# Optimization experiments

Hardware: AMD Instinct MI355X
Metric: run time of the kernel (lower is better)

Reference implementation:

```python
import jax, jax.numpy as jnp
import numpy as np

EMBED_DIM = 768
NUM_HEADS = 12
HEAD_DIM = EMBED_DIM // NUM_HEADS
B, S = 2, 2048


def setup_inputs() -> dict:
    key = jax.random.key(0)
    ks = jax.random.split(key, 6)
    glorot = jnp.sqrt(6.0 / (EMBED_DIM + EMBED_DIM)).astype(jnp.float32)
    x = jax.random.normal(ks[0], (B, S, EMBED_DIM), dtype=jnp.float32)
    mask = jnp.zeros((1, 1, S, S), dtype=jnp.float32)  # additive mask, 0 = no masking
    Wq = jax.random.uniform(ks[1], (EMBED_DIM, EMBED_DIM), jnp.float32, -glorot, glorot)
    Wk = jax.random.uniform(ks[2], (EMBED_DIM, EMBED_DIM), jnp.float32, -glorot, glorot)
    Wv = jax.random.uniform(ks[3], (EMBED_DIM, EMBED_DIM), jnp.float32, -glorot, glorot)
    Wo = jax.random.uniform(ks[4], (EMBED_DIM, EMBED_DIM), jnp.float32, -glorot, glorot)
    bo = jnp.zeros((EMBED_DIM,), dtype=jnp.float32)
    return {"x": x, "mask": mask, "Wq": Wq, "Wk": Wk, "Wv": Wv, "Wo": Wo, "bo": bo}


def reference(x, mask, Wq, Wk, Wv, Wo, bo):
    b, s, _ = x.shape
    # Q/K/V projections (no bias), split into heads: [b, h, s, d]
    def split_heads(t):
        return t.reshape(b, s, NUM_HEADS, HEAD_DIM).transpose(0, 2, 1, 3)
    q = split_heads(x @ Wq)
    k = split_heads(x @ Wk)
    v = split_heads(x @ Wv)
    scale = 1.0 / jnp.sqrt(jnp.float32(HEAD_DIM))
    logits = jnp.einsum('bhqd,bhkd->bhqk', q, k) * scale  # [b, h, s, s]
    logits = logits + mask * (-1e9)
    weights = jax.nn.softmax(logits, axis=-1)
    attn = jnp.einsum('bhqk,bhkd->bhqd', weights, v)
    concat = attn.transpose(0, 2, 1, 3).reshape(b, s, EMBED_DIM)
    return concat @ Wo + bo
```

## Files before the change

kernel.cpp:

```cpp
#include <hip/hip_runtime.h>


typedef __bf16 bf16_t;
typedef bf16_t bf16x8 __attribute__((ext_vector_type(8)));
typedef bf16_t bf16x4 __attribute__((ext_vector_type(4)));
typedef float f32x4 __attribute__((ext_vector_type(4)));
typedef _Float16 f16x4 __attribute__((ext_vector_type(4)));
typedef __fp16 hf2 __attribute__((ext_vector_type(2)));

#define SC2 0.1803368801111137f

__device__ __forceinline__ float bf2f(unsigned short u) {
  union { unsigned int i; float f; } x;
  x.i = ((unsigned int)u) << 16;
  return x.f;
}

__device__ __forceinline__ float fexp2(float x) {
  return __builtin_amdgcn_exp2f(x);
}

__device__ __forceinline__ void glds16(const bf16_t* g, bf16_t* l) {
  __builtin_amdgcn_global_load_lds(
      (const __attribute__((address_space(1))) void*)g,
      (__attribute__((address_space(3))) void*)l, 16, 0, 0);
}

__device__ __forceinline__ int detect_bf16_flag(const unsigned short* x) {
  const int lane = threadIdx.x & 63;
  const uint4* p = (const uint4*)x;
  uint4 a = p[lane * 2];
  uint4 b = p[lane * 2 + 1];
  unsigned int w[8] = {a.x, a.y, a.z, a.w, b.x, b.y, b.z, b.w};
  unsigned int big = 0;
#pragma unroll
  for (int i = 0; i < 8; i++) {
    unsigned int e0 = (w[i] >> 7) & 0xFF, e1 = (w[i] >> 23) & 0xFF;
    big |= (e0 > 0x88u) | (e1 > 0x88u);
  }
  unsigned long long bal = __ballot(big != 0u);
  return bal == 0ULL ? 1 : 0;
}

__global__ void k_prep(const void* __restrict__ x, const void* __restrict__ mask,
                       const void* __restrict__ Wq, const void* __restrict__ Wk,
                       const void* __restrict__ Wv, const void* __restrict__ Wo,
                       bf16_t* __restrict__ xb, bf16_t* __restrict__ wqkvT,
                       bf16_t* __restrict__ woT, int* __restrict__ mflags) {
  __shared__ float ts[32][33];
  __shared__ int snz;
  const int blk = blockIdx.x;
  const int f = detect_bf16_flag((const unsigned short*)x);

  if (blk < 1536) {
    if (f) return;
    int i = blk * 256 + threadIdx.x;
    const float* xf = (const float*)x + (size_t)i * 8;
    bf16x8 v;
#pragma unroll
    for (int j = 0; j < 8; j++) v[j] = (bf16_t)xf[j];
    *(bf16x8*)(xb + (size_t)i * 8) = v;
  } else if (blk < 3840) {
    const int t = blk - 1536;
    const int z = t / 576, r = t % 576, kt = r / 24, nt = r % 24;
    const void* wsrc = (z == 0) ? Wq : (z == 1) ? Wk : (z == 2) ? Wv : Wo;
    bf16_t* dst = (z < 3) ? (wqkvT + (size_t)z * 768 * 768) : woT;
    const int c = threadIdx.x & 31, r0 = threadIdx.x >> 5;
#pragma unroll
    for (int i = 0; i < 4; i++) {
      int kr = kt * 32 + r0 + i * 8;
      float v;
      if (f) v = bf2f(((const unsigned short*)wsrc)[(size_t)kr * 768 + nt * 32 + c]);
      else   v = ((const float*)wsrc)[(size_t)kr * 768 + nt * 32 + c];
      ts[r0 + i * 8][c] = v;
    }
    __syncthreads();
#pragma unroll
    for (int i = 0; i < 4; i++) {
      int nr = nt * 32 + r0 + i * 8;
      dst[(size_t)nr * 768 + kt * 32 + c] = (bf16_t)ts[c][r0 + i * 8];
    }
  } else {
    const int t = blk - 3840;
    const int qt = t >> 4, ktm = t & 15;
    if (threadIdx.x == 0) snz = 0;
    __syncthreads();
    unsigned int nz = 0;
    if (f) {
#pragma unroll
      for (int i = 0; i < 8; i++) {
        int uidx = i * 256 + threadIdx.x;
        int row = uidx >> 4, col = uidx & 15;
        const uint4* p = (const uint4*)((const char*)mask +
            ((size_t)(qt * 128 + row) * 2048 + ktm * 128) * 2 + col * 16);
        uint4 v = *p;
        nz |= ((v.x | v.y | v.z | v.w) & 0x7fff7fffu);
      }
    } else {
#pragma unroll
      for (int i = 0; i < 16; i++) {
        int uidx = i * 256 + threadIdx.x;
        int row = uidx >> 5, col = uidx & 31;
        const uint4* p = (const uint4*)((const char*)mask +
            ((size_t)(qt * 128 + row) * 2048 + ktm * 128) * 4 + col * 16);
        uint4 v = *p;
        nz |= ((v.x | v.y | v.z | v.w) & 0x7fffffffu);
      }
    }
    if (nz) snz = 1;
    __syncthreads();
    if (threadIdx.x == 0) mflags[qt * 16 + ktm] = snz;
  }
}

__global__ __launch_bounds__(256, 3) void k_gemmQKV(
    const bf16_t* __restrict__ xb, const bf16_t* __restrict__ Bm,
    bf16_t* __restrict__ Qd, bf16_t* __restrict__ Kd, _Float16* __restrict__ Vt,
    const unsigned short* __restrict__ xdet) {
  __shared__ __align__(16) char smem[32768];
  _Float16* Tb = (_Float16*)smem;

  const int f = detect_bf16_flag(xdet);
  const bf16_t* A = f ? (const bf16_t*)xdet : xb;

  const int tid = threadIdx.x;
  const int n0 = blockIdx.x * 128, m0 = blockIdx.y * 128;
  const int r = tid >> 2, c8 = (tid & 3) << 3;
  const bf16_t* Ag = A + (size_t)(m0 + r) * 768 + c8;
  const bf16_t* Bg = Bm + (size_t)(n0 + r) * 768 + c8;
  const int wid = tid >> 6, lane = tid & 63;
  const int wm = (wid >> 1) << 6, wn = (wid & 1) << 6;
  const int lr = lane & 15, lk = (lane >> 4) << 3, g4 = (lane >> 4) << 2;

  f32x4 acc[4][4];
  const f32x4 z = {0.f, 0.f, 0.f, 0.f};
#pragma unroll
  for (int i = 0; i < 4; i++)
#pragma unroll
    for (int j = 0; j < 4; j++) acc[i][j] = z;

  {
    bf16_t* A0 = (bf16_t*)smem;
    bf16_t* B0 = (bf16_t*)(smem + 16384);
    glds16(Ag, A0 + wid * 512);
    glds16(Ag + (size_t)64 * 768, A0 + 2048 + wid * 512);
    glds16(Bg, B0 + wid * 512);
    glds16(Bg + (size_t)64 * 768, B0 + 2048 + wid * 512);
  }
  __syncthreads();

  for (int s = 0; s < 24; s++) {
    if (s < 23) {
      const int k0 = (s + 1) * 32;
      bf16_t* An = (bf16_t*)(smem + ((s + 1) & 1) * 8192);
      bf16_t* Bn = (bf16_t*)(smem + 16384 + ((s + 1) & 1) * 8192);
      glds16(Ag + k0, An + wid * 512);
      glds16(Ag + (size_t)64 * 768 + k0, An + 2048 + wid * 512);
      glds16(Bg + k0, Bn + wid * 512);
      glds16(Bg + (size_t)64 * 768 + k0, Bn + 2048 + wid * 512);
    }
    const bf16_t* As = (const bf16_t*)(smem + (s & 1) * 8192);
    const bf16_t* Bs = (const bf16_t*)(smem + 16384 + (s & 1) * 8192);
    bf16x8 af[4], bf_[4];
#pragma unroll
    for (int t = 0; t < 4; t++) af[t]  = *(const bf16x8*)&As[(wm + t * 16 + lr) * 32 + lk];
#pragma unroll
    for (int t = 0; t < 4; t++) bf_[t] = *(const bf16x8*)&Bs[(wn + t * 16 + lr) * 32 + lk];
#pragma unroll
    for (int i = 0; i < 4; i++)
#pragma unroll
      for (int j = 0; j < 4; j++)
        acc[i][j] = __builtin_amdgcn_mfma_f32_16x16x32_bf16(af[i], bf_[j], acc[i][j], 0, 0, 0);
    __syncthreads();
  }

  if (n0 < 1536) {
    bf16_t* dst = (n0 < 768) ? Qd : Kd;
    const int nb = (n0 < 768) ? n0 : n0 - 768;
    const int bb = m0 >> 11;
#pragma unroll
    for (int i = 0; i < 4; i++)
#pragma unroll
      for (int j = 0; j < 4; j++) {
        const int rc = nb + wn + j * 16 + lr;
        const int hh = rc >> 6, dd = rc & 63;
        const size_t base = (((size_t)bb * 12 + hh) * 2048) * 64 + dd;
#pragma unroll
        for (int reg = 0; reg < 4; reg++) {
          const int s = (m0 & 2047) + wm + i * 16 + g4 + reg;
          dst[base + (size_t)s * 64] = (bf16_t)acc[i][j][reg];
        }
      }
  } else {
    const int bb = m0 >> 11;
#pragma unroll
    for (int half = 0; half < 2; half++) {
      if ((wid & 1) == half) {
#pragma unroll
        for (int j = 0; j < 4; j++) {
          const int d_l = j * 16 + lr;
#pragma unroll
          for (int i = 0; i < 4; i++)
#pragma unroll
            for (int reg = 0; reg < 4; reg++)
              Tb[d_l * 136 + wm + i * 16 + g4 + reg] = (_Float16)acc[i][j][reg];
        }
      }
      __syncthreads();
      const int row = tid >> 2, cc = (tid & 3) * 32;
      const int vcol = (n0 - 1536) + half * 64 + row;
      const int hh = vcol >> 6;
      _Float16* dstv = Vt + (((size_t)bb * 12 + hh) * 64 + row) * 2048 + (m0 & 2047) + cc;
#pragma unroll
      for (int u = 0; u < 4; u++)
        *(uint4*)(dstv + u * 8) = *(const uint4*)&Tb[row * 136 + cc + u * 8];
      __syncthreads();
    }
  }
}

__global__ __launch_bounds__(320, 4) void k_flash(
    const bf16_t* __restrict__ Qd, const bf16_t* __restrict__ Kd,
    const _Float16* __restrict__ Vt, const void* __restrict__ mask,
    const int* __restrict__ mflags, const unsigned short* __restrict__ xdet,
    bf16_t* __restrict__ attn) {
  __shared__ __align__(16) char sm[32768];

  const int tid = threadIdx.x, wid = tid >> 6, lane = tid & 63;
  const int lr = lane & 15, quad = lane >> 4, lk = quad << 3, g4 = quad << 2;

  const int lin = blockIdx.x;
  const int gx = lin & 7, ww = lin >> 3;
  const int hb = gx * 3 + (ww >> 5);
  const int h = hb % 12, bb = hb / 12;
  const int qt = ww & 31;

  const size_t bh = (size_t)bb * 12 + h;
  const char* Kh = (const char*)(Kd + bh * 2048 * 64);
  const char* Vh = (const char*)(Vt + bh * 64 * 2048);

  if (wid == 4) {
    const char* kS[8]; const char* vS[8];
#pragma unroll
    for (int u = 0; u < 8; u++) {
      const int R = (u >> 1) * 16 + lr;
      const int c = (u & 1) * 4 + quad;
      kS[u] = Kh + R * 128 + c * 16;
      const int u2 = u * 2 + (lane >> 5);
      const int dtv = u2 & 3, ctv = u2 >> 2, j2 = lane & 31;
      vS[u] = Vh + (size_t)(dtv * 16 + (j2 & 15)) * 4096 + ctv * 32 + (j2 >> 4) * 16;
    }
    uint4 kv[8], vv[8];
#pragma unroll
    for (int u = 0; u < 8; u++) kv[u] = *(const uint4*)(kS[u]);
#pragma unroll
    for (int u = 0; u < 8; u++) vv[u] = *(const uint4*)(vS[u]);
#pragma unroll
    for (int u = 0; u < 8; u++) *(uint4*)(sm + u * 1024 + lane * 16) = kv[u];
#pragma unroll
    for (int u = 0; u < 8; u++) *(uint4*)(sm + 8192 + u * 1024 + lane * 16) = vv[u];
    __syncthreads();
    for (int s = 0; s < 32; s++) {
      if (s < 31) {
        const int t = s + 1;
        char* buf = sm + (t & 1) * 16384;
#pragma unroll
        for (int u = 0; u < 8; u++) kv[u] = *(const uint4*)(kS[u] + (size_t)t * 8192);
#pragma unroll
        for (int u = 0; u < 8; u++) vv[u] = *(const uint4*)(vS[u] + (size_t)t * 128);
#pragma unroll
        for (int u = 0; u < 8; u++) *(uint4*)(buf + u * 1024 + lane * 16) = kv[u];
#pragma unroll
        for (int u = 0; u < 8; u++) *(uint4*)(buf + 8192 + u * 1024 + lane * 16) = vv[u];
      }
      __syncthreads();
    }
    return;
  }

  const bf16_t* Qh = Qd + bh * 2048 * 64;
  const int q0 = qt * 64 + wid * 16;
  const int mbf = detect_bf16_flag(xdet);
  const int* mfrow = mflags + (qt >> 1) * 16;
  int mbits = 0;
#pragma unroll
  for (int t = 0; t < 16; t++) mbits |= (mfrow[t] != 0) << t;

  const bf16x8 qf0 = *(const bf16x8*)&Qh[(size_t)(q0 + lr) * 64 + lk];
  const bf16x8 qf1 = *(const bf16x8*)&Qh[(size_t)(q0 + lr) * 64 + 32 + lk];

  f16x4 ones;
  ones[0] = (_Float16)1.f; ones[1] = (_Float16)1.f;
  ones[2] = (_Float16)1.f; ones[3] = (_Float16)1.f;

  const f32x4 z = {0.f, 0.f, 0.f, 0.f};
  f32x4 ot[4];
#pragma unroll
  for (int dt = 0; dt < 4; dt++) ot[dt] = z;
  float mrow = -1e30f, lrow = 0.f;

  __syncthreads();

  for (int s = 0; s < 32; s++) {
    const char* Kc = sm + (s & 1) * 16384;
    const char* Vc = Kc + 8192;

    f32x4 sv[4];
#pragma unroll
    for (int ct = 0; ct < 4; ct++) sv[ct] = z;
#pragma unroll
    for (int ct = 0; ct < 4; ct++) {
      bf16x8 kf0 = *(const bf16x8*)(Kc + ct * 2048 + lane * 16);
      bf16x8 kf1 = *(const bf16x8*)(Kc + ct * 2048 + 1024 + lane * 16);
      sv[ct] = __builtin_amdgcn_mfma_f32_16x16x32_bf16(kf0, qf0, sv[ct], 0, 0, 0);
      sv[ct] = __builtin_amdgcn_mfma_f32_16x16x32_bf16(kf1, qf1, sv[ct], 0, 0, 0);
    }

    if ((mbits >> (s >> 1)) & 1) {
#pragma unroll
      for (int ct = 0; ct < 4; ct++)
#pragma unroll
        for (int reg = 0; reg < 4; reg++) {
          size_t mi = (size_t)(q0 + lr) * 2048 + s * 64 + ct * 16 + g4 + reg;
          float mv = mbf ? bf2f(((const unsigned short*)mask)[mi])
                         : ((const float*)mask)[mi];
          sv[ct][reg] -= 8e9f * mv;
        }
    }

    float t = fmaxf(
        fmaxf(fmaxf(fmaxf(sv[0][0], sv[0][1]), fmaxf(sv[0][2], sv[0][3])),
              fmaxf(fmaxf(sv[1][0], sv[1][1]), fmaxf(sv[1][2], sv[1][3]))),
        fmaxf(fmaxf(fmaxf(sv[2][0], sv[2][1]), fmaxf(sv[2][2], sv[2][3])),
              fmaxf(fmaxf(sv[3][0], sv[3][1]), fmaxf(sv[3][2], sv[3][3]))));
    t = fmaxf(t, __shfl_xor(t, 16));
    t = fmaxf(t, __shfl_xor(t, 32));
    const float mnew = fmaxf(mrow, t);
    if (__ballot(mnew > mrow)) {
      const float alpha = fexp2((mrow - mnew) * SC2);
#pragma unroll
      for (int dt = 0; dt < 4; dt++)
#pragma unroll
        for (int reg = 0; reg < 4; reg++) ot[dt][reg] *= alpha;
      lrow *= alpha;
    }
    mrow = mnew;
    const float mS = mnew * SC2;

    f16x4 pb[4];
#pragma unroll
    for (int ct = 0; ct < 4; ct++) {
      float p0 = fexp2(fmaf(sv[ct][0], SC2, -mS));
      float p1 = fexp2(fmaf(sv[ct][1], SC2, -mS));
      float p2 = fexp2(fmaf(sv[ct][2], SC2, -mS));
      float p3 = fexp2(fmaf(sv[ct][3], SC2, -mS));
      union { hf2 h[2]; f16x4 v; } u;
      u.h[0] = __builtin_amdgcn_cvt_pkrtz(p0, p1);
      u.h[1] = __builtin_amdgcn_cvt_pkrtz(p2, p3);
      pb[ct] = u.v;
    }

    f32x4 asum = z;
#pragma unroll
    for (int ct = 0; ct < 4; ct++) {
      asum = __builtin_amdgcn_mfma_f32_16x16x16f16(ones, pb[ct], asum, 0, 0, 0);
#pragma unroll
      for (int dt = 0; dt < 4; dt++) {
        f16x4 va = *(const f16x4*)(Vc + (ct * 4 + dt) * 512 +
                                   (quad >> 1) * 256 + lr * 16 + (quad & 1) * 8);
        ot[dt] = __builtin_amdgcn_mfma_f32_16x16x16f16(va, pb[ct], ot[dt], 0, 0, 0);
      }
    }
    lrow += asum[0];
    __syncthreads();
  }

  const float inv = 1.0f / lrow;
  bf16_t* arow = attn + ((size_t)bb * 2048 + q0 + lr) * 768 + h * 64 + g4;
#pragma unroll
  for (int dt = 0; dt < 4; dt++) {
    bf16x4 v;
#pragma unroll
    for (int reg = 0; reg < 4; reg++) v[reg] = (bf16_t)(ot[dt][reg] * inv);
    *(bf16x4*)(arow + dt * 16) = v;
  }
}

__global__ __launch_bounds__(256, 3) void k_gemm2(
    const bf16_t* __restrict__ A, const bf16_t* __restrict__ Bm,
    const void* __restrict__ bo, const unsigned short* __restrict__ xdet,
    float* __restrict__ outF, unsigned short* __restrict__ outH) {
  __shared__ __align__(16) char smem[32768];

  const int tid = threadIdx.x, wid = tid >> 6, lane = tid & 63;
  const int n0 = blockIdx.x * 64, m0 = blockIdx.y * 64;
  const int wm = (wid >> 1) << 5, wn = (wid & 1) << 5;
  const int lr = lane & 15, lk = (lane >> 4) << 3, g4 = (lane >> 4) << 2;
  const bf16_t* Ag = A + (size_t)(m0 + (tid >> 2)) * 768 + ((tid & 3) << 3);
  const bf16_t* Bg = Bm + (size_t)(n0 + (tid >> 2)) * 768 + ((tid & 3) << 3);

  f32x4 acc[2][2];
  const f32x4 z = {0.f, 0.f, 0.f, 0.f};
#pragma unroll
  for (int i = 0; i < 2; i++)
#pragma unroll
    for (int j = 0; j < 2; j++) acc[i][j] = z;

  {
    bf16_t* A0 = (bf16_t*)smem;
    bf16_t* B0 = (bf16_t*)(smem + 16384);
    glds16(Ag, A0 + wid * 512);
    glds16(Ag + 32, A0 + 2048 + wid * 512);
    glds16(Bg, B0 + wid * 512);
    glds16(Bg + 32, B0 + 2048 + wid * 512);
  }
  __syncthreads();

  for (int s = 0; s < 12; s++) {
    if (s < 11) {
      const int k0 = (s + 1) * 64;
      bf16_t* An = (bf16_t*)(smem + ((s + 1) & 1) * 8192);
      bf16_t* Bn = (bf16_t*)(smem + 16384 + ((s + 1) & 1) * 8192);
      glds16(Ag + k0, An + wid * 512);
      glds16(Ag + k0 + 32, An + 2048 + wid * 512);
      glds16(Bg + k0, Bn + wid * 512);
      glds16(Bg + k0 + 32, Bn + 2048 + wid * 512);
    }
#pragma unroll
    for (int kc = 0; kc < 2; kc++) {
      const bf16_t* As = (const bf16_t*)(smem + (s & 1) * 8192) + kc * 2048;
      const bf16_t* Bs = (const bf16_t*)(smem + 16384 + (s & 1) * 8192) + kc * 2048;
      bf16x8 af[2], bf_[2];
#pragma unroll
      for (int i = 0; i < 2; i++) af[i]  = *(const bf16x8*)&As[(wm + i * 16 + lr) * 32 + lk];
#pragma unroll
      for (int j = 0; j < 2; j++) bf_[j] = *(const bf16x8*)&Bs[(wn + j * 16 + lr) * 32 + lk];
#pragma unroll
      for (int i = 0; i < 2; i++)
#pragma unroll
        for (int j = 0; j < 2; j++)
          acc[i][j] = __builtin_amdgcn_mfma_f32_16x16x32_bf16(af[i], bf_[j], acc[i][j], 0, 0, 0);
    }
    __syncthreads();
  }

  const int obf = detect_bf16_flag(xdet);
#pragma unroll
  for (int i = 0; i < 2; i++)
#pragma unroll
    for (int j = 0; j < 2; j++) {
      const int nn = n0 + wn + j * 16 + lr;
      const float bv = obf ? bf2f(((const unsigned short*)bo)[nn])
                           : ((const float*)bo)[nn];
#pragma unroll
      for (int reg = 0; reg < 4; reg++) {
        const int m = m0 + wm + i * 16 + g4 + reg;
        const float v = acc[i][j][reg] + bv;
        if (obf) outH[(size_t)m * 768 + nn] = __builtin_bit_cast(unsigned short, (bf16_t)v);
        else     outF[(size_t)m * 768 + nn] = v;
      }
    }
}

extern "C" void kernel_launch(void* const* d_in, const int* in_sizes, int n_in,
                              void* d_out, int out_size, void* d_ws, size_t ws_size,
                              hipStream_t stream) {
  (void)in_sizes; (void)n_in; (void)out_size; (void)ws_size;
  const void* x    = d_in[0];
  const void* mask = d_in[1];
  const void* Wq   = d_in[2];
  const void* Wk   = d_in[3];
  const void* Wv   = d_in[4];
  const void* Wo   = d_in[5];
  const void* bo   = d_in[6];

  char* w = (char*)d_ws;
  size_t off = 0;
  auto take = [&](size_t b) -> void* {
    void* p = w + off;
    off = (off + b + 255) & ~(size_t)255;
    return p;
  };
  int*      mflags = (int*)take(256 * 4);
  bf16_t*   wqkvT  = (bf16_t*)take((size_t)2304 * 768 * 2);
  bf16_t*   woT    = (bf16_t*)take((size_t)768 * 768 * 2);
  bf16_t*   xb     = (bf16_t*)take((size_t)4096 * 768 * 2);
  bf16_t*   Qd     = (bf16_t*)take((size_t)3145728 * 2);
  bf16_t*   Kd     = (bf16_t*)take((size_t)3145728 * 2);
  _Float16* Vt     = (_Float16*)take((size_t)3145728 * 2);
  bf16_t*   attn   = xb;

  k_prep<<<4096, 256, 0, stream>>>(x, mask, Wq, Wk, Wv, Wo, xb, wqkvT, woT, mflags);
  k_gemmQKV<<<dim3(18, 32), 256, 0, stream>>>(xb, wqkvT, Qd, Kd, Vt,
                                              (const unsigned short*)x);
  k_flash<<<768, 320, 0, stream>>>(Qd, Kd, Vt, mask, mflags,
                                   (const unsigned short*)x, attn);
  k_gemm2<<<dim3(12, 64), 256, 0, stream>>>(attn, woT, bo, (const unsigned short*)x,
                                            (float*)d_out, (unsigned short*)d_out);
}
```

Before: 179.3 us.

## Use 16x16x32 f16 MFMA for PV with permuted K/swizzled V LDS layout

Reorganizes how the producer wave stores K and V tiles in LDS. K rows are permuted so each lane's score registers line up with eight contiguous keys, and V is stored row-major with an XOR swizzle. This lets the P·V and row-sum products use the wider 16x16x32 f16 MFMA with f16x8 operands, halving the number of MFMA and LDS read instructions. It also defers the online-softmax rescale until the row max grows past a threshold, and raises wave priority around the MFMA blocks. The deferred rescale relies on exp values staying within f16 range, and the mask indexing is adjusted to match the new key permutation.

```diff
diff --git a/kernel.cpp b/kernel.cpp
--- a/kernel.cpp
+++ b/kernel.cpp
@@ -6,9 +6,11 @@
 typedef bf16_t bf16x4 __attribute__((ext_vector_type(4)));
 typedef float f32x4 __attribute__((ext_vector_type(4)));
 typedef _Float16 f16x4 __attribute__((ext_vector_type(4)));
+typedef _Float16 f16x8 __attribute__((ext_vector_type(8)));
 typedef __fp16 hf2 __attribute__((ext_vector_type(2)));
 
 #define SC2 0.1803368801111137f
+#define DEFER_THR 44.0f
 
 __device__ __forceinline__ float bf2f(unsigned short u) {
   union { unsigned int i; float f; } x;
@@ -241,14 +243,17 @@
 
   if (wid == 4) {
     const char* kS[8]; const char* vS[8];
+    int kL[8], vL[8];
 #pragma unroll
     for (int u = 0; u < 8; u++) {
       const int R = (u >> 1) * 16 + lr;
-      const int c = (u & 1) * 4 + quad;
-      kS[u] = Kh + R * 128 + c * 16;
-      const int u2 = u * 2 + (lane >> 5);
-      const int dtv = u2 & 3, ctv = u2 >> 2, j2 = lane & 31;
-      vS[u] = Vh + (size_t)(dtv * 16 + (j2 & 15)) * 4096 + ctv * 32 + (j2 >> 4) * 16;
+      const int cG = (u & 1) * 4 + quad;
+      kS[u] = Kh + R * 128 + cG * 16;
+      const int s = ((u >> 2) << 5) + (((lr >> 2) & 1) << 4) +
+                    (((u >> 1) & 1) << 3) + ((lr >> 3) << 2) + (lr & 3);
+      kL[u] = (s >> 4) * 2048 + (cG & 3) * 256 + (s & 15) * 16 + (cG >> 2) * 1024;
+      vS[u] = Vh + (size_t)lane * 4096 + u * 16;
+      vL[u] = 8192 + lane * 128 + ((u * 16) ^ ((lane & 7) << 4));
     }
     uint4 kv[8], vv[8];
 #pragma unroll
@@ -256,9 +261,9 @@
 #pragma unroll
     for (int u = 0; u < 8; u++) vv[u] = *(const uint4*)(vS[u]);
 #pragma unroll
-    for (int u = 0; u < 8; u++) *(uint4*)(sm + u * 1024 + lane * 16) = kv[u];
-#pragma unroll
-    for (int u = 0; u < 8; u++) *(uint4*)(sm + 8192 + u * 1024 + lane * 16) = vv[u];
+    for (int u = 0; u < 8; u++) *(uint4*)(sm + kL[u]) = kv[u];
+#pragma unroll
+    for (int u = 0; u < 8; u++) *(uint4*)(sm + vL[u]) = vv[u];
     __syncthreads();
     for (int s = 0; s < 32; s++) {
       if (s < 31) {
@@ -269,9 +274,9 @@
 #pragma unroll
         for (int u = 0; u < 8; u++) vv[u] = *(const uint4*)(vS[u] + (size_t)t * 128);
 #pragma unroll
-        for (int u = 0; u < 8; u++) *(uint4*)(buf + u * 1024 + lane * 16) = kv[u];
-#pragma unroll
-        for (int u = 0; u < 8; u++) *(uint4*)(buf + 8192 + u * 1024 + lane * 16) = vv[u];
+        for (int u = 0; u < 8; u++) *(uint4*)(buf + kL[u]) = kv[u];
+#pragma unroll
+        for (int u = 0; u < 8; u++) *(uint4*)(buf + vL[u]) = vv[u];
       }
       __syncthreads();
     }
@@ -289,9 +294,12 @@
   const bf16x8 qf0 = *(const bf16x8*)&Qh[(size_t)(q0 + lr) * 64 + lk];
   const bf16x8 qf1 = *(const bf16x8*)&Qh[(size_t)(q0 + lr) * 64 + 32 + lk];
 
-  f16x4 ones;
-  ones[0] = (_Float16)1.f; ones[1] = (_Float16)1.f;
-  ones[2] = (_Float16)1.f; ones[3] = (_Float16)1.f;
+  f16x8 ones8;
+#pragma unroll
+  for (int j = 0; j < 8; j++) ones8[j] = (_Float16)1.f;
+
+  const int vxo0 = (quad * 16) ^ ((lr & 7) << 4);
+  const int vxo1 = (64 + quad * 16) ^ ((lr & 7) << 4);
 
   const f32x4 z = {0.f, 0.f, 0.f, 0.f};
   f32x4 ot[4];
@@ -308,6 +316,7 @@
     f32x4 sv[4];
 #pragma unroll
     for (int ct = 0; ct < 4; ct++) sv[ct] = z;
+    __builtin_amdgcn_s_setprio(1);
 #pragma unroll
     for (int ct = 0; ct < 4; ct++) {
       bf16x8 kf0 = *(const bf16x8*)(Kc + ct * 2048 + lane * 16);
@@ -315,13 +324,15 @@
       sv[ct] = __builtin_amdgcn_mfma_f32_16x16x32_bf16(kf0, qf0, sv[ct], 0, 0, 0);
       sv[ct] = __builtin_amdgcn_mfma_f32_16x16x32_bf16(kf1, qf1, sv[ct], 0, 0, 0);
     }
+    __builtin_amdgcn_s_setprio(0);
 
     if ((mbits >> (s >> 1)) & 1) {
 #pragma unroll
       for (int ct = 0; ct < 4; ct++)
 #pragma unroll
         for (int reg = 0; reg < 4; reg++) {
-          size_t mi = (size_t)(q0 + lr) * 2048 + s * 64 + ct * 16 + g4 + reg;
+          const int kk = ((ct >> 1) << 5) + (quad << 3) + ((ct & 1) << 2) + reg;
+          size_t mi = (size_t)(q0 + lr) * 2048 + s * 64 + kk;
           float mv = mbf ? bf2f(((const unsigned short*)mask)[mi])
                          : ((const float*)mask)[mi];
           sv[ct][reg] -= 8e9f * mv;
@@ -335,42 +346,48 @@
               fmaxf(fmaxf(sv[3][0], sv[3][1]), fmaxf(sv[3][2], sv[3][3]))));
     t = fmaxf(t, __shfl_xor(t, 16));
     t = fmaxf(t, __shfl_xor(t, 32));
-    const float mnew = fmaxf(mrow, t);
-    if (__ballot(mnew > mrow)) {
+    if (__ballot(t > mrow + DEFER_THR)) {
+      const float mnew = fmaxf(mrow, t);
       const float alpha = fexp2((mrow - mnew) * SC2);
 #pragma unroll
       for (int dt = 0; dt < 4; dt++)
 #pragma unroll
         for (int reg = 0; reg < 4; reg++) ot[dt][reg] *= alpha;
       lrow *= alpha;
-    }
-    mrow = mnew;
-    const float mS = mnew * SC2;
-
-    f16x4 pb[4];
-#pragma unroll
-    for (int ct = 0; ct < 4; ct++) {
-      float p0 = fexp2(fmaf(sv[ct][0], SC2, -mS));
-      float p1 = fexp2(fmaf(sv[ct][1], SC2, -mS));
-      float p2 = fexp2(fmaf(sv[ct][2], SC2, -mS));
-      float p3 = fexp2(fmaf(sv[ct][3], SC2, -mS));
-      union { hf2 h[2]; f16x4 v; } u;
-      u.h[0] = __builtin_amdgcn_cvt_pkrtz(p0, p1);
-      u.h[1] = __builtin_amdgcn_cvt_pkrtz(p2, p3);
-      pb[ct] = u.v;
+      mrow = mnew;
+    }
+    const float mS = mrow * SC2;
+
+    f16x8 pb8[2];
+#pragma unroll
+    for (int c2 = 0; c2 < 2; c2++) {
+      union { hf2 h[4]; f16x8 v; } u;
+#pragma unroll
+      for (int hh2 = 0; hh2 < 2; hh2++) {
+        const int ct = c2 * 2 + hh2;
+        float p0 = fexp2(fmaf(sv[ct][0], SC2, -mS));
+        float p1 = fexp2(fmaf(sv[ct][1], SC2, -mS));
+        float p2 = fexp2(fmaf(sv[ct][2], SC2, -mS));
+        float p3 = fexp2(fmaf(sv[ct][3], SC2, -mS));
+        u.h[hh2 * 2 + 0] = __builtin_amdgcn_cvt_pkrtz(p0, p1);
+        u.h[hh2 * 2 + 1] = __builtin_amdgcn_cvt_pkrtz(p2, p3);
+      }
+      pb8[c2] = u.v;
     }
 
     f32x4 asum = z;
-#pragma unroll
-    for (int ct = 0; ct < 4; ct++) {
-      asum = __builtin_amdgcn_mfma_f32_16x16x16f16(ones, pb[ct], asum, 0, 0, 0);
+    __builtin_amdgcn_s_setprio(1);
+#pragma unroll
+    for (int c2 = 0; c2 < 2; c2++) {
+      const int vxo = c2 ? vxo1 : vxo0;
+      asum = __builtin_amdgcn_mfma_f32_16x16x32_f16(ones8, pb8[c2], asum, 0, 0, 0);
 #pragma unroll
       for (int dt = 0; dt < 4; dt++) {
-        f16x4 va = *(const f16x4*)(Vc + (ct * 4 + dt) * 512 +
-                                   (quad >> 1) * 256 + lr * 16 + (quad & 1) * 8);
-        ot[dt] = __builtin_amdgcn_mfma_f32_16x16x16f16(va, pb[ct], ot[dt], 0, 0, 0);
-      }
-    }
+        f16x8 va = *(const f16x8*)(Vc + (dt * 16 + lr) * 128 + vxo);
+        ot[dt] = __builtin_amdgcn_mfma_f32_16x16x32_f16(va, pb8[c2], ot[dt], 0, 0, 0);
+      }
+    }
+    __builtin_amdgcn_s_setprio(0);
     lrow += asum[0];
     __syncthreads();
   }
```

Result: no change. 178.1 us (-0.7%).
